# Performance work log

Measured on AMD Instinct MI355X. Metric: run time of the kernel, lower is better.

The kernel has to match this reference:

```python
import jax, jax.numpy as jnp
import numpy as np

B, S, T = 32, 64, 48
E = 128          # embed size
H = 256          # encoder hidden (per direction)
HD = 512         # decoder hidden = 2*H
V = 32001        # vocab_size + 1


def setup_inputs() -> dict:
    key = jax.random.key(0)
    ks = jax.random.split(key, 20)
    p = lambda k, shp: jax.random.normal(k, shp, dtype=jnp.float32) * 0.05
    inp = {}
    inp["input_sequence"] = jax.random.randint(ks[0], (B, S), 0, V)
    lengths = jax.random.randint(ks[1], (B,), 1, S + 1).at[0].set(S)
    inp["input_seq_lengths"] = lengths
    inp["output_sequence"] = jax.random.randint(ks[2], (B, T), 0, V)
    # encoder params
    inp["emb_src"] = p(ks[3], (V, E))
    inp["Wih_f"] = p(ks[4], (4 * H, E)); inp["Whh_f"] = p(ks[5], (4 * H, H)); inp["b_f"] = p(ks[6], (4 * H,))
    inp["Wih_b"] = p(ks[7], (4 * H, E)); inp["Whh_b"] = p(ks[8], (4 * H, H)); inp["b_b"] = p(ks[9], (4 * H,))
    # decoder params
    inp["emb_tgt"] = p(ks[10], (V, E))
    inp["Wih_d"] = p(ks[11], (4 * HD, E)); inp["Whh_d"] = p(ks[12], (4 * HD, HD)); inp["b_d"] = p(ks[13], (4 * HD,))
    inp["W1"] = p(ks[14], (HD, HD)); inp["W2"] = p(ks[15], (HD, HD)); inp["v"] = p(ks[16], (HD,))
    inp["Wo"] = p(ks[17], (V, HD)); inp["bo"] = p(ks[18], (V,))
    return inp


def _cell(x, h, c, Wih, Whh, b):
    # PyTorch LSTM gate order: i, f, g, o. b = b_ih + b_hh.
    g = x @ Wih.T + h @ Whh.T + b
    i, f, gg, o = jnp.split(g, 4, axis=-1)
    c = jax.nn.sigmoid(f) * c + jax.nn.sigmoid(i) * jnp.tanh(gg)
    h = jax.nn.sigmoid(o) * jnp.tanh(c)
    return h, c


def reference(input_sequence, input_seq_lengths, output_sequence,
              emb_src, Wih_f, Whh_f, b_f, Wih_b, Whh_b, b_b,
              emb_tgt, Wih_d, Whh_d, b_d, W1, W2, v, Wo, bo):
    x = emb_src[input_sequence]                       # [B,S,E]
    valid = jnp.arange(S)[None, :] < input_seq_lengths[:, None]  # [B,S]
    xs = jnp.swapaxes(x, 0, 1)                        # [S,B,E]
    vs = valid.T                                      # [S,B]
    z = jnp.zeros((B, H), jnp.float32)

    def fstep(carry, inp):
        h, c = carry
        xt, vt = inp
        h, c = _cell(xt, h, c, Wih_f, Whh_f, b_f)
        return (h, c), jnp.where(vt[:, None], h, 0.0)

    _, of = jax.lax.scan(fstep, (z, z), (xs, vs))

    def bstep(carry, inp):
        # backward direction of a packed LSTM: state starts at each sequence's
        # last valid token (state held at zero while t >= length)
        h, c = carry
        xt, vt = inp
        hn, cn = _cell(xt, h, c, Wih_b, Whh_b, b_b)
        m = vt[:, None]
        h = jnp.where(m, hn, h)
        c = jnp.where(m, cn, c)
        return (h, c), jnp.where(m, h, 0.0)

    _, ob = jax.lax.scan(bstep, (z, z), (xs[::-1], vs[::-1]))
    ob = ob[::-1]
    enc = jnp.swapaxes(jnp.concatenate([of, ob], axis=-1), 0, 1)  # [B,S,512], zeros at pads

    key_proj = enc @ W1.T                             # precompute W1(key): [B,S,512]

    tgt_emb = emb_tgt[output_sequence]                # [B,T,E]
    dec_in = jnp.concatenate([jnp.zeros((B, 1, E), jnp.float32), tgt_emb[:, :-1]], axis=1)
    dec_xs = jnp.swapaxes(dec_in, 0, 1)               # [T,B,E]

    def dstep(carry, xt):
        h, c = carry
        h, c = _cell(xt, h, c, Wih_d, Whh_d, b_d)
        qp = h @ W2.T                                 # [B,512]
        energy = jnp.tanh(key_proj + qp[:, None, :]) @ v   # [B,S]
        energy = jnp.where(valid, energy, -1e10)
        w = jax.nn.softmax(energy, axis=1)
        ctx = jnp.einsum('bs,bsd->bd', w, enc)        # [B,512]
        logits = (h + ctx) @ Wo.T + bo                # [B,V]
        return (h, c), logits

    z2 = jnp.zeros((B, HD), jnp.float32)
    _, logits = jax.lax.scan(dstep, (z2, z2), dec_xs)
    outputs = jnp.swapaxes(logits, 0, 1)              # [B,T,V]

    # CrossEntropyLoss(ignore_index=0), mean over non-ignored targets
    logp = jax.nn.log_softmax(outputs, axis=-1)
    nll = -jnp.take_along_axis(logp, output_sequence[:, :, None], axis=-1)[..., 0]
    m = (output_sequence != 0).astype(jnp.float32)
    loss = jnp.sum(nll * m) / jnp.maximum(jnp.sum(m), 1.0)
    return outputs, loss
```

## Files before the change

kernel.cpp:

```cpp
#include <hip/hip_runtime.h>


typedef unsigned short ushort_t;
typedef unsigned int   uint_t;
typedef unsigned long long ull_t;
typedef __attribute__((ext_vector_type(8))) short bf16x8;
typedef __attribute__((ext_vector_type(4))) float f32x4;

#define DEV static __device__ __forceinline__

#define NB 32
#define NS 64
#define NT 48
#define NE 128
#define NH 256
#define ND 512
#define NV 32001

#define OFF_GF   0ull
#define OFF_GB   8388608ull
#define OFF_GD   16777216ull
#define OFF_KP   29360128ull
#define OFF_CWO  0ull
#define OFF_QP   33554432ull
#define OFF_ENC  36700160ull
#define OFF_HBF  38797312ull
#define OFF_ACTX 40370176ull
#define OFF_XEE  41943040ull
#define OFF_XED  42467328ull
#define OFF_CWF  42860544ull
#define OFF_CWB  43122688ull
#define OFF_CWD  43384832ull
#define OFF_CW1  43909120ull
#define OFF_CW2  44433408ull
#define OFF_HBE  44957696ull
#define OFF_HBD  45023232ull
#define OFF_MISC 45088768ull

DEV float b2f(ushort_t u) { return __uint_as_float(((uint_t)u) << 16); }
DEV ushort_t f2b(float f) {
  uint_t x = __float_as_uint(f);
  return (ushort_t)((x + 0x7fffu + ((x >> 16) & 1u)) >> 16);
}
DEV float fsig(float x) { return 1.f / (1.f + __expf(-x)); }
DEV float ftanh(float x) { float e = __expf(2.f * x); return 1.f - 2.f / (e + 1.f); }

DEV f32x4 mfma16(bf16x8 a, bf16x8 b, f32x4 c) {
  return __builtin_amdgcn_mfma_f32_16x16x32_bf16(a, b, c, 0, 0, 0);
}
DEV void async16(void* lds, const void* g) {
  __builtin_amdgcn_global_load_lds(
      (const __attribute__((address_space(1))) uint_t*)g,
      (__attribute__((address_space(3))) uint_t*)lds, 16, 0, 0);
}
DEV bf16x8 ldw8(const float* p) {
  f32x4 a = *(const f32x4*)p;
  f32x4 b = *(const f32x4*)(p + 4);
  bf16x8 r;
  r[0] = (short)f2b(a[0]); r[1] = (short)f2b(a[1]);
  r[2] = (short)f2b(a[2]); r[3] = (short)f2b(a[3]);
  r[4] = (short)f2b(b[0]); r[5] = (short)f2b(b[1]);
  r[6] = (short)f2b(b[2]); r[7] = (short)f2b(b[3]);
  return r;
}

DEV void st8_cc(void* p, ull_t v) {
  __hip_atomic_store((ull_t*)p, v, __ATOMIC_RELAXED, __HIP_MEMORY_SCOPE_AGENT);
}
DEV ull_t ld8_cc(const void* p) {
  return __hip_atomic_load((ull_t*)p, __ATOMIC_RELAXED, __HIP_MEMORY_SCOPE_AGENT);
}

__global__ void init_ws(uint_t* misc) {
  for (int i = threadIdx.x; i < 1024; i += 256) misc[i] = 0u;
}

__global__ __launch_bounds__(256) void cvt_bf16(const float* __restrict__ src,
                                                ushort_t* __restrict__ dst,
                                                int n4) {
  int i = blockIdx.x * 256 + threadIdx.x;
  if (i < n4) {
    f32x4 x = *(const f32x4*)(src + (size_t)i * 4);
    uint_t lo = ((uint_t)f2b(x[1]) << 16) | (uint_t)f2b(x[0]);
    uint_t hi = ((uint_t)f2b(x[3]) << 16) | (uint_t)f2b(x[2]);
    uint2 v; v.x = lo; v.y = hi;
    *(uint2*)(dst + (size_t)i * 4) = v;
  }
}

__global__ __launch_bounds__(128) void gather_enc(const float* __restrict__ emb,
                                                  const int* __restrict__ seq,
                                                  ushort_t* __restrict__ xe) {
  int m = blockIdx.x;
  int s = m >> 5, b = m & 31;
  int tok = seq[b * NS + s];
  xe[(size_t)m * NE + threadIdx.x] = f2b(emb[(size_t)tok * NE + threadIdx.x]);
}
__global__ __launch_bounds__(128) void gather_dec(const float* __restrict__ emb,
                                                  const int* __restrict__ seq,
                                                  ushort_t* __restrict__ xe) {
  int m = blockIdx.x;
  int t = m >> 5, b = m & 31;
  float v = 0.f;
  if (t > 0) v = emb[(size_t)seq[b * NT + t - 1] * NE + threadIdx.x];
  xe[(size_t)m * NE + threadIdx.x] = f2b(v);
}

template <int CMODE, int BIAS>
__global__ __launch_bounds__(256, 2) void gemm_nt(
    const ushort_t* __restrict__ Abase, const ushort_t* __restrict__ Bmat,
    const float* __restrict__ bias, float* __restrict__ Cf,
    int N, int K, int Nvalid) {
  const int tid = threadIdx.x;
  const int wv = tid >> 6, l = tid & 63, c15 = l & 15, q = l >> 4;
  const int mw = wv >> 1, nw = wv & 1;
  const int n0 = blockIdx.x * 128, m0 = blockIdx.y * 128;
  __shared__ __align__(16) ushort_t lds[32 * 512];

  f32x4 acc[4][4];
  const f32x4 zz = {0.f, 0.f, 0.f, 0.f};
#pragma unroll
  for (int i = 0; i < 4; ++i)
#pragma unroll
    for (int j = 0; j < 4; ++j) acc[i][j] = zz;

  for (int k0 = 0; k0 < K; k0 += 64) {
    __syncthreads();
#pragma unroll
    for (int i = 0; i < 4; ++i) {
      const int slot = wv * 4 + i;
      const int kt = slot >> 3, mt = slot & 7;
      const int m = m0 + mt * 16 + c15;
      async16(&lds[slot * 512], Abase + (size_t)m * K + k0 + kt * 32 + q * 8);
      int n = n0 + mt * 16 + c15;
      if (n >= Nvalid) n = Nvalid - 1;
      async16(&lds[(16 + slot) * 512], Bmat + (size_t)n * K + k0 + kt * 32 + q * 8);
    }
    __syncthreads();
#pragma unroll
    for (int kt = 0; kt < 2; ++kt) {
      bf16x8 af[4], bfr[4];
#pragma unroll
      for (int i = 0; i < 4; ++i)
        af[i] = *(const bf16x8*)&lds[(kt * 8 + mw * 4 + i) * 512 + l * 8];
#pragma unroll
      for (int i = 0; i < 4; ++i)
        bfr[i] = *(const bf16x8*)&lds[(16 + kt * 8 + nw * 4 + i) * 512 + l * 8];
#pragma unroll
      for (int mi = 0; mi < 4; ++mi)
#pragma unroll
        for (int ni = 0; ni < 4; ++ni)
          acc[mi][ni] = mfma16(af[mi], bfr[ni], acc[mi][ni]);
    }
  }
#pragma unroll
  for (int mi = 0; mi < 4; ++mi)
#pragma unroll
    for (int ni = 0; ni < 4; ++ni) {
      const int n = n0 + (nw * 4 + ni) * 16 + c15;
      float bv = 0.f;
      if (BIAS) { if (CMODE != 2 || n < Nvalid) bv = bias[n]; }
#pragma unroll
      for (int r = 0; r < 4; ++r) {
        const int m = m0 + (mw * 4 + mi) * 16 + q * 4 + r;
        const float val = acc[mi][ni][r] + bv;
        if (CMODE == 0) Cf[(size_t)m * N + n] = val;
        else if (CMODE == 1) Cf[((size_t)(m >> 5) * N + n) * 32 + (m & 31)] = val;
        else if (n < Nvalid) Cf[(size_t)m * (size_t)NV + n] = val;
      }
    }
}

__global__ __launch_bounds__(512, 2) void enc_scan(
    const float* __restrict__ WhhF, const float* __restrict__ WhhB,
    const float* __restrict__ gF, const float* __restrict__ gB,
    const int* __restrict__ lens, ushort_t* __restrict__ enc_bf,
    ushort_t* __restrict__ hbuf, int* __restrict__ flags) {
  const int tid = threadIdx.x;
  const int d = blockIdx.x >> 1, p = blockIdx.x & 1;
  const int w = tid >> 6, l = tid & 63, c = l & 15, q = l >> 4;
  const float* Whh = d ? WhhB : WhhF;
  const float* gpre = d ? gB : gF;
  ushort_t* hb_base = hbuf + (size_t)d * 2 * 8192;
  int* flag = flags + d * 16;
  const int u = p * 128 + w * 16 + c;

  bf16x8 wf[4][8];
#pragma unroll
  for (int g = 0; g < 4; ++g)
#pragma unroll
    for (int kt = 0; kt < 8; ++kt)
      wf[g][kt] = ldw8(Whh + (size_t)(g * 256 + u) * 256 + kt * 32 + q * 8);

  __shared__ __align__(16) ushort_t hsh[2][8192];
  for (int i = tid; i < 8192; i += 512) hsh[0][i] = 0;
  float cst[8], hst[8];
#pragma unroll
  for (int i = 0; i < 8; ++i) { cst[i] = 0.f; hst[i] = 0.f; }
  int lensr[8];
#pragma unroll
  for (int mt = 0; mt < 2; ++mt)
#pragma unroll
    for (int r = 0; r < 4; ++r) lensr[mt * 4 + r] = lens[mt * 16 + q * 4 + r];
  const int kt_u = u >> 5, j_u = u & 7, hi16 = ((u >> 3) & 3) << 4;

  f32x4 gv[4][2];
  {
    const int so0 = d ? 63 : 0;
#pragma unroll
    for (int g = 0; g < 4; ++g) {
      const float* gp = gpre + ((size_t)so0 * 1024 + (g * 256 + u)) * 32 + q * 4;
      gv[g][0] = *(const f32x4*)gp;
      gv[g][1] = *(const f32x4*)(gp + 16);
    }
  }
  __syncthreads();

  int tgt = 0;
#pragma unroll 1
  for (int s = 0; s < 64; ++s) {
    const int so = d ? (63 - s) : s;
    const int rb = s & 1, nb = rb ^ 1;
    f32x4 acc[4][2];
#pragma unroll
    for (int g = 0; g < 4; ++g) { acc[g][0] = gv[g][0]; acc[g][1] = gv[g][1]; }
    if (s < 63) {
      const int son = d ? (62 - s) : (s + 1);
#pragma unroll
      for (int g = 0; g < 4; ++g) {
        const float* gp = gpre + ((size_t)son * 1024 + (g * 256 + u)) * 32 + q * 4;
        gv[g][0] = *(const f32x4*)gp;
        gv[g][1] = *(const f32x4*)(gp + 16);
      }
    }
#pragma unroll
    for (int kt = 0; kt < 8; ++kt) {
      bf16x8 a0 = *(const bf16x8*)&hsh[rb][kt * 512 + l * 8];
      bf16x8 a1 = *(const bf16x8*)&hsh[rb][(8 + kt) * 512 + l * 8];
#pragma unroll
      for (int g = 0; g < 4; ++g) {
        acc[g][0] = mfma16(a0, wf[g][kt], acc[g][0]);
        acc[g][1] = mfma16(a1, wf[g][kt], acc[g][1]);
      }
    }
#pragma unroll
    for (int mt = 0; mt < 2; ++mt)
#pragma unroll
      for (int r = 0; r < 4; ++r) {
        const int k8 = mt * 4 + r;
        const int bi = mt * 16 + q * 4 + r;
        float gi = acc[0][mt][r], gf = acc[1][mt][r];
        float gg = acc[2][mt][r], go = acc[3][mt][r];
        float ctn = fsig(gf) * cst[k8] + fsig(gi) * ftanh(gg);
        float hn = fsig(go) * ftanh(ctn);
        bool valid = so < lensr[k8];
        bool upd = (d == 0) || valid;
        cst[k8] = upd ? ctn : cst[k8];
        hst[k8] = upd ? hn : hst[k8];
        enc_bf[((size_t)bi * 64 + so) * 512 + d * 256 + u] = f2b(valid ? hn : 0.f);
        hsh[nb][((mt * 8 + kt_u) * 64 + ((bi & 15) | hi16)) * 8 + j_u] =
            f2b(hst[k8]);
      }
    if (s == 63) break;
    __syncthreads();

    ushort_t* hbw = hb_base + nb * 8192;
    {
      ull_t* gdst = (ull_t*)hbw;
      const ull_t* lsrc = (const ull_t*)&hsh[nb][0];
#pragma unroll
      for (int mt2 = 0; mt2 < 2; ++mt2) {
        const int base = (mt2 * 8 + 4 * p) * 128;
        st8_cc(gdst + base + tid, lsrc[base + tid]);
      }
    }
    asm volatile("s_waitcnt vmcnt(0)" ::: "memory");
    __syncthreads();
    tgt += 2;
    if (tid == 0) {
      __hip_atomic_fetch_add(flag, 1, __ATOMIC_RELAXED, __HIP_MEMORY_SCOPE_AGENT);
      while (__hip_atomic_load(flag, __ATOMIC_RELAXED, __HIP_MEMORY_SCOPE_AGENT) < tgt)
        __builtin_amdgcn_s_sleep(1);
    }
    __syncthreads();
    {
      const ull_t* gsrc = (const ull_t*)hbw;
#pragma unroll
      for (int mt2 = 0; mt2 < 2; ++mt2) {
        const int base = (mt2 * 8 + 4 * (1 - p)) * 128;
        ull_t v = ld8_cc(gsrc + base + tid);
        ((ull_t*)&hsh[nb][0])[base + tid] = v;
      }
    }
    __syncthreads();
  }
}

__global__ __launch_bounds__(512, 2) void dec_scan(
    const float* __restrict__ Whh, const float* __restrict__ gpre,
    ushort_t* __restrict__ h_bf, ushort_t* __restrict__ hbuf,
    int* __restrict__ flag) {
  const int tid = threadIdx.x;
  const int bb = blockIdx.x;
  const int w = tid >> 6, l = tid & 63, c = l & 15, q = l >> 4;
  const int uu = bb * 64 + w * 8 + (c & 7);
  const int row0 = ((c >> 3)) * 512 + uu;
  const int row1 = (2 + (c >> 3)) * 512 + uu;

  bf16x8 wf0[16], wf1[16];
#pragma unroll
  for (int kt = 0; kt < 16; ++kt) {
    wf0[kt] = ldw8(Whh + (size_t)row0 * 512 + kt * 32 + q * 8);
    wf1[kt] = ldw8(Whh + (size_t)row1 * 512 + kt * 32 + q * 8);
  }
  __shared__ __align__(16) ushort_t hsh[2][16384];
  for (int i = tid; i < 16384; i += 512) hsh[0][i] = 0;
  float cst[8];
#pragma unroll
  for (int i = 0; i < 8; ++i) cst[i] = 0.f;
  const int kt_u = uu >> 5, j_u = uu & 7, hi16 = ((uu >> 3) & 3) << 4;

  f32x4 ga[2], gb[2];
  {
    const float* p0 = gpre + (size_t)row0 * 32 + q * 4;
    const float* p1 = gpre + (size_t)row1 * 32 + q * 4;
    ga[0] = *(const f32x4*)p0; ga[1] = *(const f32x4*)(p0 + 16);
    gb[0] = *(const f32x4*)p1; gb[1] = *(const f32x4*)(p1 + 16);
  }
  __syncthreads();

  int tgt = 0;
#pragma unroll 1
  for (int t = 0; t < 48; ++t) {
    const int rb = t & 1, nb = rb ^ 1;
    f32x4 acc[2][2];
    acc[0][0] = ga[0]; acc[0][1] = ga[1];
    acc[1][0] = gb[0]; acc[1][1] = gb[1];
    if (t < 47) {
      const float* p0 = gpre + ((size_t)(t + 1) * 2048 + row0) * 32 + q * 4;
      const float* p1 = gpre + ((size_t)(t + 1) * 2048 + row1) * 32 + q * 4;
      ga[0] = *(const f32x4*)p0; ga[1] = *(const f32x4*)(p0 + 16);
      gb[0] = *(const f32x4*)p1; gb[1] = *(const f32x4*)(p1 + 16);
    }
#pragma unroll
    for (int kt = 0; kt < 16; ++kt) {
      bf16x8 a0 = *(const bf16x8*)&hsh[rb][kt * 512 + l * 8];
      bf16x8 a1 = *(const bf16x8*)&hsh[rb][(16 + kt) * 512 + l * 8];
      acc[0][0] = mfma16(a0, wf0[kt], acc[0][0]);
      acc[0][1] = mfma16(a1, wf0[kt], acc[0][1]);
      acc[1][0] = mfma16(a0, wf1[kt], acc[1][0]);
      acc[1][1] = mfma16(a1, wf1[kt], acc[1][1]);
    }
#pragma unroll
    for (int mt = 0; mt < 2; ++mt)
#pragma unroll
      for (int r = 0; r < 4; ++r) {
        const int k8 = mt * 4 + r;
        const int bi = mt * 16 + q * 4 + r;
        float x0 = acc[0][mt][r];
        float x1 = acc[1][mt][r];
        float Av = fsig(x0) * ftanh(x1);
        float Ar = __shfl_xor(Av, 8, 64);
        if (c >= 8) {
          float ctn = fsig(x0) * cst[k8] + Ar;
          float hn = fsig(x1) * ftanh(ctn);
          cst[k8] = ctn;
          ushort_t hb16 = f2b(hn);
          h_bf[((size_t)t * 32 + bi) * 512 + uu] = hb16;
          hsh[nb][((mt * 16 + kt_u) * 64 + ((bi & 15) | hi16)) * 8 + j_u] = hb16;
        }
      }
    if (t == 47) break;
    __syncthreads();

    ushort_t* hbw = hbuf + nb * 16384;
    {
      const int chunk = tid >> 7, word = tid & 127;
      const int mt = chunk >> 1, ktl = chunk & 1;
      const size_t off = ((size_t)(mt * 16 + bb * 2 + ktl) * 512) + (size_t)word * 4;
      ull_t v = *(const ull_t*)&hsh[nb][off];
      st8_cc(hbw + off, v);
    }
    asm volatile("s_waitcnt vmcnt(0)" ::: "memory");
    __syncthreads();
    tgt += 8;
    if (tid == 0) {
      __hip_atomic_fetch_add(flag, 1, __ATOMIC_RELAXED, __HIP_MEMORY_SCOPE_AGENT);
      while (__hip_atomic_load(flag, __ATOMIC_RELAXED, __HIP_MEMORY_SCOPE_AGENT) < tgt)
        __builtin_amdgcn_s_sleep(1);
    }
    __syncthreads();
    {
      ull_t tv[8];
#pragma unroll
      for (int j = 0; j < 8; ++j)
        tv[j] = ld8_cc((const ull_t*)hbw + tid + j * 512);
#pragma unroll
      for (int j = 0; j < 8; ++j)
        ((ull_t*)&hsh[nb][0])[tid + j * 512] = tv[j];
    }
    __syncthreads();
  }
}

__global__ __launch_bounds__(256) void attn_k(
    const float* __restrict__ qp, const float* __restrict__ kp,
    const ushort_t* __restrict__ enc_bf, const ushort_t* __restrict__ h_bf,
    const float* __restrict__ vvec, const int* __restrict__ lens,
    ushort_t* __restrict__ actx) {
  const int bid = blockIdx.x;
  const int b = bid / NT, t = bid % NT;
  const int tid = threadIdx.x;
  __shared__ float qps[512], vs[512], es[64];
  {
    const float* qrow = qp + ((size_t)t * 32 + b) * 512;
    float2 x = *(const float2*)&qrow[tid * 2];
    qps[tid * 2] = x.x; qps[tid * 2 + 1] = x.y;
    float2 vv = *(const float2*)&vvec[tid * 2];
    vs[tid * 2] = vv.x; vs[tid * 2 + 1] = vv.y;
  }
  __syncthreads();
  const int s = tid >> 2, i = tid & 3;
  const int len = lens[b];
  {
    const float* kr = kp + ((size_t)b * 64 + s) * 512 + i * 128;
    float e = 0.f;
#pragma unroll 8
    for (int k = 0; k < 128; k += 4) {
      f32x4 x = *(const f32x4*)&kr[k];
      const int ko = i * 128 + k;
      e += ftanh(x[0] + qps[ko]) * vs[ko];
      e += ftanh(x[1] + qps[ko + 1]) * vs[ko + 1];
      e += ftanh(x[2] + qps[ko + 2]) * vs[ko + 2];
      e += ftanh(x[3] + qps[ko + 3]) * vs[ko + 3];
    }
    e += __shfl_xor(e, 1, 64);
    e += __shfl_xor(e, 2, 64);
    if (i == 0) es[s] = (s < len) ? e : -1e10f;
  }
  __syncthreads();
  if (tid < 64) {
    float x = es[tid], m = x;
#pragma unroll
    for (int o = 1; o < 64; o <<= 1) m = fmaxf(m, __shfl_xor(m, o, 64));
    float pe = __expf(x - m), sum = pe;
#pragma unroll
    for (int o = 1; o < 64; o <<= 1) sum += __shfl_xor(sum, o, 64);
    es[tid] = pe / sum;
  }
  __syncthreads();
  const int d0 = tid * 2;
  float a0 = 0.f, a1 = 0.f;
  const ushort_t* erow = enc_bf + (size_t)b * 64 * 512 + d0;
#pragma unroll 4
  for (int ss = 0; ss < 64; ++ss) {
    uint_t uv = *(const uint_t*)(erow + (size_t)ss * 512);
    float wgt = es[ss];
    a0 += wgt * b2f((ushort_t)(uv & 0xffff));
    a1 += wgt * b2f((ushort_t)(uv >> 16));
  }
  uint_t hu = *(const uint_t*)(h_bf + ((size_t)t * 32 + b) * 512 + d0);
  float o0 = a0 + b2f((ushort_t)(hu & 0xffff));
  float o1 = a1 + b2f((ushort_t)(hu >> 16));
  uint_t packed = ((uint_t)f2b(o1) << 16) | (uint_t)f2b(o0);
  *(uint_t*)(actx + ((size_t)b * NT + t) * 512 + d0) = packed;
}

__global__ __launch_bounds__(256) void loss_k(const float* __restrict__ outp,
                                              const int* __restrict__ oseq,
                                              float* __restrict__ acc) {
  const int m = blockIdx.x;
  const int b = m / NT, t = m % NT;
  const int tid = threadIdx.x;
  const float* row = outp + (size_t)m * NV;
  __shared__ float redM[4], redS[4];
  float mx = -1e30f, sm = 0.f;
  for (int v = tid; v < NV; v += 256) {
    float x = row[v];
    float m2 = fmaxf(mx, x);
    sm = sm * __expf(mx - m2) + __expf(x - m2);
    mx = m2;
  }
#pragma unroll
  for (int o = 1; o < 64; o <<= 1) {
    float mo = __shfl_xor(mx, o, 64);
    float so = __shfl_xor(sm, o, 64);
    float m2 = fmaxf(mx, mo);
    sm = sm * __expf(mx - m2) + so * __expf(mo - m2);
    mx = m2;
  }
  if ((tid & 63) == 0) { redM[tid >> 6] = mx; redS[tid >> 6] = sm; }
  __syncthreads();
  if (tid == 0) {
    float M = redM[0], S = redS[0];
#pragma unroll
    for (int i = 1; i < 4; ++i) {
      float m2 = fmaxf(M, redM[i]);
      S = S * __expf(M - m2) + redS[i] * __expf(redM[i] - m2);
      M = m2;
    }
    float lse = __logf(S) + M;
    int tok = oseq[b * NT + t];
    float nll = lse - row[tok];
    if (tok != 0) { atomicAdd(&acc[0], nll); atomicAdd(&acc[1], 1.f); }
  }
}

__global__ void finalize_loss(const float* __restrict__ acc,
                              float* __restrict__ outp) {
  if (threadIdx.x == 0)
    outp[(size_t)NB * NT * NV] = acc[0] / fmaxf(acc[1], 1.f);
}

extern "C" void kernel_launch(void* const* d_in, const int* in_sizes, int n_in,
                              void* d_out, int out_size, void* d_ws,
                              size_t ws_size, hipStream_t stream) {
  (void)in_sizes; (void)n_in; (void)out_size; (void)ws_size;
  const int* in_seq  = (const int*)d_in[0];
  const int* lens    = (const int*)d_in[1];
  const int* out_seq = (const int*)d_in[2];
  const float* emb_src = (const float*)d_in[3];
  const float* Wih_f = (const float*)d_in[4];
  const float* Whh_f = (const float*)d_in[5];
  const float* b_f   = (const float*)d_in[6];
  const float* Wih_b = (const float*)d_in[7];
  const float* Whh_b = (const float*)d_in[8];
  const float* b_b   = (const float*)d_in[9];
  const float* emb_tgt = (const float*)d_in[10];
  const float* Wih_d = (const float*)d_in[11];
  const float* Whh_d = (const float*)d_in[12];
  const float* b_d   = (const float*)d_in[13];
  const float* W1 = (const float*)d_in[14];
  const float* W2 = (const float*)d_in[15];
  const float* vv = (const float*)d_in[16];
  const float* Wo = (const float*)d_in[17];
  const float* bo = (const float*)d_in[18];

  char* ws = (char*)d_ws;
  float* g_fT    = (float*)(ws + OFF_GF);
  float* g_bT    = (float*)(ws + OFF_GB);
  float* g_dT    = (float*)(ws + OFF_GD);
  float* keyp    = (float*)(ws + OFF_KP);
  float* qp      = (float*)(ws + OFF_QP);
  ushort_t* encb = (ushort_t*)(ws + OFF_ENC);
  ushort_t* hbf  = (ushort_t*)(ws + OFF_HBF);
  ushort_t* actx = (ushort_t*)(ws + OFF_ACTX);
  ushort_t* xee  = (ushort_t*)(ws + OFF_XEE);
  ushort_t* xed  = (ushort_t*)(ws + OFF_XED);
  ushort_t* c_wf = (ushort_t*)(ws + OFF_CWF);
  ushort_t* c_wb = (ushort_t*)(ws + OFF_CWB);
  ushort_t* c_wd = (ushort_t*)(ws + OFF_CWD);
  ushort_t* c_w1 = (ushort_t*)(ws + OFF_CW1);
  ushort_t* c_w2 = (ushort_t*)(ws + OFF_CW2);
  ushort_t* c_wo = (ushort_t*)(ws + OFF_CWO);
  ushort_t* hbe  = (ushort_t*)(ws + OFF_HBE);
  ushort_t* hbd  = (ushort_t*)(ws + OFF_HBD);
  int* flags     = (int*)(ws + OFF_MISC);
  float* accp    = (float*)(ws + OFF_MISC + 256);
  float* outp    = (float*)d_out;

  init_ws<<<1, 256, 0, stream>>>((uint_t*)(ws + OFF_MISC));
  gather_enc<<<NB * NS, 128, 0, stream>>>(emb_src, in_seq, xee);
  gather_dec<<<NB * NT, 128, 0, stream>>>(emb_tgt, out_seq, xed);
  cvt_bf16<<<128, 256, 0, stream>>>(Wih_f, c_wf, 32768);
  cvt_bf16<<<128, 256, 0, stream>>>(Wih_b, c_wb, 32768);
  cvt_bf16<<<256, 256, 0, stream>>>(Wih_d, c_wd, 65536);
  cvt_bf16<<<256, 256, 0, stream>>>(W1, c_w1, 65536);
  cvt_bf16<<<256, 256, 0, stream>>>(W2, c_w2, 65536);
  gemm_nt<1, 1><<<dim3(8, 16), 256, 0, stream>>>(
      xee, c_wf, b_f, g_fT, 1024, 128, 1024);
  gemm_nt<1, 1><<<dim3(8, 16), 256, 0, stream>>>(
      xee, c_wb, b_b, g_bT, 1024, 128, 1024);
  gemm_nt<1, 1><<<dim3(16, 12), 256, 0, stream>>>(
      xed, c_wd, b_d, g_dT, 2048, 128, 2048);
  enc_scan<<<4, 512, 0, stream>>>(Whh_f, Whh_b, g_fT, g_bT, lens, encb, hbe,
                                  flags);
  gemm_nt<0, 0><<<dim3(4, 16), 256, 0, stream>>>(
      encb, c_w1, nullptr, keyp, 512, 512, 512);
  dec_scan<<<8, 512, 0, stream>>>(Whh_d, g_dT, hbf, hbd, flags + 32);
  gemm_nt<0, 0><<<dim3(4, 12), 256, 0, stream>>>(
      hbf, c_w2, nullptr, qp, 512, 512, 512);
  attn_k<<<NB * NT, 256, 0, stream>>>(qp, keyp, encb, hbf, vv, lens, actx);
  cvt_bf16<<<16001, 256, 0, stream>>>(Wo, c_wo, 4096128);
  gemm_nt<2, 1><<<dim3(251, 12), 256, 0, stream>>>(
      actx, c_wo, bo, outp, NV, 512, NV);
  loss_k<<<NB * NT, 256, 0, stream>>>(outp, out_seq, accp);
  finalize_loss<<<1, 64, 0, stream>>>(accp, outp);
}
```

Measured before the change: 1.341 ms.

## Replace shared atomic counters with per-block flags and overlap recurrent scan work

The encoder and decoder recurrent scans stop using one shared fetch-add counter that every block spins on. Each block now publishes its step in its own flag, and waiters poll only their peers' flags: one wavefront-wide poll in the decoder, a single peer in the encoder. In the encoder, the MFMA half that uses the block's own freshly computed hidden state runs before waiting for the peer's half, and output stores plus gate-preactivation prefetch move into the wait window. This aims to hide inter-block barrier latency on the serial critical path, at the cost of more complex flag handling and a larger flag region in the workspace.

```diff
diff --git a/kernel.cpp b/kernel.cpp
--- a/kernel.cpp
+++ b/kernel.cpp
@@ -70,6 +70,12 @@
 DEV ull_t ld8_cc(const void* p) {
   return __hip_atomic_load((ull_t*)p, __ATOMIC_RELAXED, __HIP_MEMORY_SCOPE_AGENT);
 }
+DEV void st32_cc(int* p, int v) {
+  __hip_atomic_store(p, v, __ATOMIC_RELAXED, __HIP_MEMORY_SCOPE_AGENT);
+}
+DEV int ld32_cc(const int* p) {
+  return __hip_atomic_load(p, __ATOMIC_RELAXED, __HIP_MEMORY_SCOPE_AGENT);
+}
 
 __global__ void init_ws(uint_t* misc) {
   for (int i = threadIdx.x; i < 1024; i += 256) misc[i] = 0u;
@@ -182,8 +188,10 @@
   const float* Whh = d ? WhhB : WhhF;
   const float* gpre = d ? gB : gF;
   ushort_t* hb_base = hbuf + (size_t)d * 2 * 8192;
-  int* flag = flags + d * 16;
+  int* flag_self = flags + (d * 2 + p) * 16;
+  int* flag_peer = flags + (d * 2 + (1 - p)) * 16;
   const int u = p * 128 + w * 16 + c;
+  const int kt0_own = p * 4, kt0_peer = (1 - p) * 4;
 
   bf16x8 wf[4][8];
 #pragma unroll
@@ -204,37 +212,26 @@
     for (int r = 0; r < 4; ++r) lensr[mt * 4 + r] = lens[mt * 16 + q * 4 + r];
   const int kt_u = u >> 5, j_u = u & 7, hi16 = ((u >> 3) & 3) << 4;
 
-  f32x4 gv[4][2];
+  f32x4 acc[4][2], gv[4][2];
   {
-    const int so0 = d ? 63 : 0;
+    const int so0 = d ? 63 : 0, so1 = d ? 62 : 1;
 #pragma unroll
     for (int g = 0; g < 4; ++g) {
-      const float* gp = gpre + ((size_t)so0 * 1024 + (g * 256 + u)) * 32 + q * 4;
-      gv[g][0] = *(const f32x4*)gp;
-      gv[g][1] = *(const f32x4*)(gp + 16);
+      const float* g0 = gpre + ((size_t)so0 * 1024 + (g * 256 + u)) * 32 + q * 4;
+      const float* g1 = gpre + ((size_t)so1 * 1024 + (g * 256 + u)) * 32 + q * 4;
+      acc[g][0] = *(const f32x4*)g0; acc[g][1] = *(const f32x4*)(g0 + 16);
+      gv[g][0] = *(const f32x4*)g1; gv[g][1] = *(const f32x4*)(g1 + 16);
     }
   }
   __syncthreads();
 
-  int tgt = 0;
 #pragma unroll 1
   for (int s = 0; s < 64; ++s) {
     const int so = d ? (63 - s) : s;
     const int rb = s & 1, nb = rb ^ 1;
-    f32x4 acc[4][2];
-#pragma unroll
-    for (int g = 0; g < 4; ++g) { acc[g][0] = gv[g][0]; acc[g][1] = gv[g][1]; }
-    if (s < 63) {
-      const int son = d ? (62 - s) : (s + 1);
-#pragma unroll
-      for (int g = 0; g < 4; ++g) {
-        const float* gp = gpre + ((size_t)son * 1024 + (g * 256 + u)) * 32 + q * 4;
-        gv[g][0] = *(const f32x4*)gp;
-        gv[g][1] = *(const f32x4*)(gp + 16);
-      }
-    }
-#pragma unroll
-    for (int kt = 0; kt < 8; ++kt) {
+#pragma unroll
+    for (int j = 0; j < 4; ++j) {
+      const int kt = kt0_peer + j;
       bf16x8 a0 = *(const bf16x8*)&hsh[rb][kt * 512 + l * 8];
       bf16x8 a1 = *(const bf16x8*)&hsh[rb][(8 + kt) * 512 + l * 8];
 #pragma unroll
@@ -257,16 +254,25 @@
         bool upd = (d == 0) || valid;
         cst[k8] = upd ? ctn : cst[k8];
         hst[k8] = upd ? hn : hst[k8];
-        enc_bf[((size_t)bi * 64 + so) * 512 + d * 256 + u] = f2b(valid ? hn : 0.f);
         hsh[nb][((mt * 8 + kt_u) * 64 + ((bi & 15) | hi16)) * 8 + j_u] =
             f2b(hst[k8]);
       }
-    if (s == 63) break;
-    __syncthreads();
-
-    ushort_t* hbw = hb_base + nb * 8192;
+    if (s == 63) {
+#pragma unroll
+      for (int mt = 0; mt < 2; ++mt)
+#pragma unroll
+        for (int r = 0; r < 4; ++r) {
+          const int k8 = mt * 4 + r;
+          const int bi = mt * 16 + q * 4 + r;
+          const bool valid = so < lensr[k8];
+          enc_bf[((size_t)bi * 64 + so) * 512 + d * 256 + u] =
+              f2b(valid ? hst[k8] : 0.f);
+        }
+      break;
+    }
+    __syncthreads();
     {
-      ull_t* gdst = (ull_t*)hbw;
+      ull_t* gdst = (ull_t*)(hb_base + nb * 8192);
       const ull_t* lsrc = (const ull_t*)&hsh[nb][0];
 #pragma unroll
       for (int mt2 = 0; mt2 < 2; ++mt2) {
@@ -274,22 +280,48 @@
         st8_cc(gdst + base + tid, lsrc[base + tid]);
       }
     }
+#pragma unroll
+    for (int g = 0; g < 4; ++g) { acc[g][0] = gv[g][0]; acc[g][1] = gv[g][1]; }
+#pragma unroll
+    for (int j = 0; j < 4; ++j) {
+      const int kt = kt0_own + j;
+      bf16x8 a0 = *(const bf16x8*)&hsh[nb][kt * 512 + l * 8];
+      bf16x8 a1 = *(const bf16x8*)&hsh[nb][(8 + kt) * 512 + l * 8];
+#pragma unroll
+      for (int g = 0; g < 4; ++g) {
+        acc[g][0] = mfma16(a0, wf[g][kt], acc[g][0]);
+        acc[g][1] = mfma16(a1, wf[g][kt], acc[g][1]);
+      }
+    }
     asm volatile("s_waitcnt vmcnt(0)" ::: "memory");
     __syncthreads();
-    tgt += 2;
-    if (tid == 0) {
-      __hip_atomic_fetch_add(flag, 1, __ATOMIC_RELAXED, __HIP_MEMORY_SCOPE_AGENT);
-      while (__hip_atomic_load(flag, __ATOMIC_RELAXED, __HIP_MEMORY_SCOPE_AGENT) < tgt)
-        __builtin_amdgcn_s_sleep(1);
-    }
-    __syncthreads();
+    if (tid == 0) st32_cc(flag_self, s + 1);
+    if (s < 62) {
+      const int son = d ? (61 - s) : (s + 2);
+#pragma unroll
+      for (int g = 0; g < 4; ++g) {
+        const float* gp = gpre + ((size_t)son * 1024 + (g * 256 + u)) * 32 + q * 4;
+        gv[g][0] = *(const f32x4*)gp;
+        gv[g][1] = *(const f32x4*)(gp + 16);
+      }
+    }
+#pragma unroll
+    for (int mt = 0; mt < 2; ++mt)
+#pragma unroll
+      for (int r = 0; r < 4; ++r) {
+        const int k8 = mt * 4 + r;
+        const int bi = mt * 16 + q * 4 + r;
+        const bool valid = so < lensr[k8];
+        enc_bf[((size_t)bi * 64 + so) * 512 + d * 256 + u] =
+            f2b(valid ? hst[k8] : 0.f);
+      }
+    while (ld32_cc(flag_peer) < s + 1) __builtin_amdgcn_s_sleep(1);
     {
-      const ull_t* gsrc = (const ull_t*)hbw;
+      const ull_t* gsrc = (const ull_t*)(hb_base + nb * 8192);
 #pragma unroll
       for (int mt2 = 0; mt2 < 2; ++mt2) {
         const int base = (mt2 * 8 + 4 * (1 - p)) * 128;
-        ull_t v = ld8_cc(gsrc + base + tid);
-        ((ull_t*)&hsh[nb][0])[base + tid] = v;
+        ((ull_t*)&hsh[nb][0])[base + tid] = ld8_cc(gsrc + base + tid);
       }
     }
     __syncthreads();
@@ -299,7 +331,7 @@
 __global__ __launch_bounds__(512, 2) void dec_scan(
     const float* __restrict__ Whh, const float* __restrict__ gpre,
     ushort_t* __restrict__ h_bf, ushort_t* __restrict__ hbuf,
-    int* __restrict__ flag) {
+    int* __restrict__ flags) {
   const int tid = threadIdx.x;
   const int bb = blockIdx.x;
   const int w = tid >> 6, l = tid & 63, c = l & 15, q = l >> 4;
@@ -320,28 +352,22 @@
   for (int i = 0; i < 8; ++i) cst[i] = 0.f;
   const int kt_u = uu >> 5, j_u = uu & 7, hi16 = ((uu >> 3) & 3) << 4;
 
-  f32x4 ga[2], gb[2];
+  f32x4 acc[2][2], ga[2], gb[2];
   {
     const float* p0 = gpre + (size_t)row0 * 32 + q * 4;
     const float* p1 = gpre + (size_t)row1 * 32 + q * 4;
-    ga[0] = *(const f32x4*)p0; ga[1] = *(const f32x4*)(p0 + 16);
-    gb[0] = *(const f32x4*)p1; gb[1] = *(const f32x4*)(p1 + 16);
+    acc[0][0] = *(const f32x4*)p0; acc[0][1] = *(const f32x4*)(p0 + 16);
+    acc[1][0] = *(const f32x4*)p1; acc[1][1] = *(const f32x4*)(p1 + 16);
+    const float* p2 = gpre + ((size_t)2048 + row0) * 32 + q * 4;
+    const float* p3 = gpre + ((size_t)2048 + row1) * 32 + q * 4;
+    ga[0] = *(const f32x4*)p2; ga[1] = *(const f32x4*)(p2 + 16);
+    gb[0] = *(const f32x4*)p3; gb[1] = *(const f32x4*)(p3 + 16);
   }
   __syncthreads();
 
-  int tgt = 0;
 #pragma unroll 1
   for (int t = 0; t < 48; ++t) {
     const int rb = t & 1, nb = rb ^ 1;
-    f32x4 acc[2][2];
-    acc[0][0] = ga[0]; acc[0][1] = ga[1];
-    acc[1][0] = gb[0]; acc[1][1] = gb[1];
-    if (t < 47) {
-      const float* p0 = gpre + ((size_t)(t + 1) * 2048 + row0) * 32 + q * 4;
-      const float* p1 = gpre + ((size_t)(t + 1) * 2048 + row1) * 32 + q * 4;
-      ga[0] = *(const f32x4*)p0; ga[1] = *(const f32x4*)(p0 + 16);
-      gb[0] = *(const f32x4*)p1; gb[1] = *(const f32x4*)(p1 + 16);
-    }
 #pragma unroll
     for (int kt = 0; kt < 16; ++kt) {
       bf16x8 a0 = *(const bf16x8*)&hsh[rb][kt * 512 + l * 8];
@@ -351,6 +377,7 @@
       acc[1][0] = mfma16(a0, wf1[kt], acc[1][0]);
       acc[1][1] = mfma16(a1, wf1[kt], acc[1][1]);
     }
+    ushort_t hb16v[8];
 #pragma unroll
     for (int mt = 0; mt < 2; ++mt)
 #pragma unroll
@@ -366,38 +393,67 @@
           float hn = fsig(x1) * ftanh(ctn);
           cst[k8] = ctn;
           ushort_t hb16 = f2b(hn);
-          h_bf[((size_t)t * 32 + bi) * 512 + uu] = hb16;
+          hb16v[k8] = hb16;
           hsh[nb][((mt * 16 + kt_u) * 64 + ((bi & 15) | hi16)) * 8 + j_u] = hb16;
         }
       }
-    if (t == 47) break;
-    __syncthreads();
-
-    ushort_t* hbw = hbuf + nb * 16384;
+    if (t == 47) {
+      if (c >= 8) {
+#pragma unroll
+        for (int mt = 0; mt < 2; ++mt)
+#pragma unroll
+          for (int r = 0; r < 4; ++r) {
+            const int k8 = mt * 4 + r;
+            const int bi = mt * 16 + q * 4 + r;
+            h_bf[((size_t)t * 32 + bi) * 512 + uu] = hb16v[k8];
+          }
+      }
+      break;
+    }
+    __syncthreads();
     {
+      ushort_t* hbw = hbuf + nb * 16384;
       const int chunk = tid >> 7, word = tid & 127;
       const int mt = chunk >> 1, ktl = chunk & 1;
-      const size_t off = ((size_t)(mt * 16 + bb * 2 + ktl) * 512) + (size_t)word * 4;
-      ull_t v = *(const ull_t*)&hsh[nb][off];
-      st8_cc(hbw + off, v);
-    }
+      const size_t off = (size_t)(mt * 16 + bb * 2 + ktl) * 128 + word;
+      st8_cc((ull_t*)hbw + off, ((const ull_t*)&hsh[nb][0])[off]);
+    }
+    acc[0][0] = ga[0]; acc[0][1] = ga[1];
+    acc[1][0] = gb[0]; acc[1][1] = gb[1];
     asm volatile("s_waitcnt vmcnt(0)" ::: "memory");
     __syncthreads();
-    tgt += 8;
-    if (tid == 0) {
-      __hip_atomic_fetch_add(flag, 1, __ATOMIC_RELAXED, __HIP_MEMORY_SCOPE_AGENT);
-      while (__hip_atomic_load(flag, __ATOMIC_RELAXED, __HIP_MEMORY_SCOPE_AGENT) < tgt)
+    if (tid == 0) st32_cc(flags + bb * 16, t + 1);
+    if (t < 46) {
+      const float* p0 = gpre + ((size_t)(t + 2) * 2048 + row0) * 32 + q * 4;
+      const float* p1 = gpre + ((size_t)(t + 2) * 2048 + row1) * 32 + q * 4;
+      ga[0] = *(const f32x4*)p0; ga[1] = *(const f32x4*)(p0 + 16);
+      gb[0] = *(const f32x4*)p1; gb[1] = *(const f32x4*)(p1 + 16);
+    }
+    if (c >= 8) {
+#pragma unroll
+      for (int mt = 0; mt < 2; ++mt)
+#pragma unroll
+        for (int r = 0; r < 4; ++r) {
+          const int k8 = mt * 4 + r;
+          const int bi = mt * 16 + q * 4 + r;
+          h_bf[((size_t)t * 32 + bi) * 512 + uu] = hb16v[k8];
+        }
+    }
+    {
+      int* fsl = flags + (l & 7) * 16;
+      const bool own = ((l & 7) == bb);
+      while (true) {
+        int v = own ? (t + 1) : ld32_cc(fsl);
+        if (__all(v >= t + 1)) break;
         __builtin_amdgcn_s_sleep(1);
-    }
-    __syncthreads();
+      }
+    }
     {
-      ull_t tv[8];
+      const ull_t* gsrc = (const ull_t*)(hbuf + nb * 16384);
+      ull_t* ldst = (ull_t*)&hsh[nb][0];
 #pragma unroll
       for (int j = 0; j < 8; ++j)
-        tv[j] = ld8_cc((const ull_t*)hbw + tid + j * 512);
-#pragma unroll
-      for (int j = 0; j < 8; ++j)
-        ((ull_t*)&hsh[nb][0])[tid + j * 512] = tv[j];
+        ldst[tid + j * 512] = ld8_cc(gsrc + tid + j * 512);
     }
     __syncthreads();
   }
@@ -556,7 +612,7 @@
   ushort_t* hbe  = (ushort_t*)(ws + OFF_HBE);
   ushort_t* hbd  = (ushort_t*)(ws + OFF_HBD);
   int* flags     = (int*)(ws + OFF_MISC);
-  float* accp    = (float*)(ws + OFF_MISC + 256);
+  float* accp    = (float*)(ws + OFF_MISC + 3072);
   float* outp    = (float*)d_out;
 
   init_ws<<<1, 256, 0, stream>>>((uint_t*)(ws + OFF_MISC));
@@ -577,7 +633,7 @@
                                   flags);
   gemm_nt<0, 0><<<dim3(4, 16), 256, 0, stream>>>(
       encb, c_w1, nullptr, keyp, 512, 512, 512);
-  dec_scan<<<8, 512, 0, stream>>>(Whh_d, g_dT, hbf, hbd, flags + 32);
+  dec_scan<<<8, 512, 0, stream>>>(Whh_d, g_dT, hbf, hbd, flags + 256);
   gemm_nt<0, 0><<<dim3(4, 12), 256, 0, stream>>>(
       hbf, c_w2, nullptr, qp, 512, 512, 512);
   attn_k<<<NB * NT, 256, 0, stream>>>(qp, keyp, encb, hbf, vv, lens, actx);
```

Result: slower. 1.761 ms (+31.3%).
